# Optimization experiments

Measured on AMD Instinct MI355X. Metric: run time of the kernel, lower is better.

Reference implementation:

```python
import jax, jax.numpy as jnp
import numpy as np

B, T, D_MODEL, H = 4, 2048, 1024, 16
D_HEAD = D_MODEL // H
THETA = 10000.0


def setup_inputs() -> dict:
    key = jax.random.key(0)
    ks = jax.random.split(key, 5)
    s = 0.02
    return {
        "x": jax.random.normal(ks[0], (B, T, D_MODEL), dtype=jnp.float32),
        "Wq": jax.random.normal(ks[1], (D_MODEL, D_MODEL), dtype=jnp.float32) * s,
        "bq": jnp.zeros((D_MODEL,), dtype=jnp.float32),
        "Wk": jax.random.normal(ks[2], (D_MODEL, D_MODEL), dtype=jnp.float32) * s,
        "bk": jnp.zeros((D_MODEL,), dtype=jnp.float32),
        "Wv": jax.random.normal(ks[3], (D_MODEL, D_MODEL), dtype=jnp.float32) * s,
        "bv": jnp.zeros((D_MODEL,), dtype=jnp.float32),
        "Wo": jax.random.normal(ks[4], (D_MODEL, D_MODEL), dtype=jnp.float32) * s,
        "bo": jnp.zeros((D_MODEL,), dtype=jnp.float32),
    }


def _rope_tables(t_len, d_head, theta):
    inv_freq = 1.0 / theta ** (jnp.arange(0, d_head, 2, dtype=jnp.float32) / d_head)
    t = jnp.arange(t_len, dtype=jnp.float32)
    freqs = jnp.einsum('i,k->ik', t, inv_freq)  # [T, d_head/2]
    return jnp.cos(freqs), jnp.sin(freqs)


def _apply_rope(x, cos, sin):
    # x: [B, H, T, d_head]; cos/sin: [T, d_head/2] broadcast over B,H
    c = cos[None, None, :, :]
    s = sin[None, None, :, :]
    x0, x1 = x[..., ::2], x[..., 1::2]
    x_rot = jnp.stack((x0 * c - x1 * s, x0 * s + x1 * c), axis=-1)
    return x_rot.reshape(x.shape)


def reference(x, Wq, bq, Wk, bk, Wv, bv, Wo, bo):
    b, t, c = x.shape
    h, dh = H, D_HEAD
    q = (x @ Wq.T + bq).reshape(b, t, h, dh).transpose(0, 2, 1, 3)
    k = (x @ Wk.T + bk).reshape(b, t, h, dh).transpose(0, 2, 1, 3)
    v = (x @ Wv.T + bv).reshape(b, t, h, dh).transpose(0, 2, 1, 3)
    cos, sin = _rope_tables(t, dh, THETA)
    q = _apply_rope(q, cos, sin)
    k = _apply_rope(k, cos, sin)
    scores = jnp.einsum('bhqd,bhkd->bhqk', q, k) / jnp.sqrt(jnp.float32(dh))
    causal = jnp.tril(jnp.ones((t, t), dtype=bool))
    scores = jnp.where(causal[None, None, :, :], scores, -jnp.inf)
    attn = jax.nn.softmax(scores, axis=-1)
    out = jnp.einsum('bhqk,bhkd->bhqd', attn, v)
    out = out.transpose(0, 2, 1, 3).reshape(b, t, c)
    return out @ Wo.T + bo
```

## Files before the change

### kernel.cpp

```cpp
#include <hip/hip_runtime.h>
#include <hip/hip_bf16.h>

#define DEV static __device__ __forceinline__
#define AS1q __attribute__((address_space(1)))
#define AS3q __attribute__((address_space(3)))

typedef __attribute__((ext_vector_type(4))) float f32x4;
typedef __attribute__((ext_vector_type(16))) float f32x16;
typedef __attribute__((ext_vector_type(8))) short short8;
typedef __attribute__((ext_vector_type(4))) unsigned short u16x4;
typedef __attribute__((ext_vector_type(4))) unsigned int u32x4;

#define NB 4
#define NT 2048
#define NDM 1024
#define NH 16
#define NDH 64
#define NM (NB * NT)

DEV float bf2f(unsigned short u) {
  union { unsigned int i; float f; } x;
  x.i = ((unsigned int)u) << 16;
  return x.f;
}
DEV unsigned short f2bf(float f) {
  __hip_bfloat16 h = __float2bfloat16(f);
  return *reinterpret_cast<unsigned short*>(&h);
}
DEV unsigned int pack2bf(float lo, float hi) {
  return ((unsigned int)f2bf(hi) << 16) | (unsigned int)f2bf(lo);
}
DEV short8 mkfrag(unsigned int w0, unsigned int w1, unsigned int w2, unsigned int w3) {
  union { u32x4 u; short8 s; } x;
  x.u[0] = w0; x.u[1] = w1; x.u[2] = w2; x.u[3] = w3;
  return x.s;
}
DEV void permswap(unsigned int& a, unsigned int& b) {
  auto r = __builtin_amdgcn_permlane32_swap(a, b, false, false);
  a = r[0]; b = r[1];
}
DEV float dpp_swap1(float v) {
  union { float f; int i; } x; x.f = v;
  int r = __builtin_amdgcn_update_dpp(0, x.i, 0xB1, 0xF, 0xF, true);
  union { int i; float f; } y; y.i = r;
  return y.f;
}

__global__ __launch_bounds__(256) void k_cvt_bf16(const float* __restrict__ in,
                                                  unsigned short* __restrict__ out,
                                                  int n8) {
  int i = blockIdx.x * 256 + threadIdx.x;
  if (i >= n8) return;
  const f32x4* p = (const f32x4*)(in + (size_t)i * 8);
  f32x4 a = p[0], b = p[1];
  short8 o;
  o[0] = (short)f2bf(a[0]); o[1] = (short)f2bf(a[1]);
  o[2] = (short)f2bf(a[2]); o[3] = (short)f2bf(a[3]);
  o[4] = (short)f2bf(b[0]); o[5] = (short)f2bf(b[1]);
  o[6] = (short)f2bf(b[2]); o[7] = (short)f2bf(b[3]);
  *(short8*)(out + (size_t)i * 8) = o;
}

__global__ __launch_bounds__(256) void k_cvt_w(const float* __restrict__ w0, const float* __restrict__ w1,
                                               const float* __restrict__ w2, const float* __restrict__ w3,
                                               unsigned short* __restrict__ o0, unsigned short* __restrict__ o1,
                                               unsigned short* __restrict__ o2, unsigned short* __restrict__ o3) {
  int i = blockIdx.x * 256 + threadIdx.x;
  int m = blockIdx.y;
  const float* in = (m == 0) ? w0 : (m == 1) ? w1 : (m == 2) ? w2 : w3;
  unsigned short* out = (m == 0) ? o0 : (m == 1) ? o1 : (m == 2) ? o2 : o3;
  const f32x4* p = (const f32x4*)(in + (size_t)i * 8);
  f32x4 a = p[0], b = p[1];
  short8 o;
  o[0] = (short)f2bf(a[0]); o[1] = (short)f2bf(a[1]);
  o[2] = (short)f2bf(a[2]); o[3] = (short)f2bf(a[3]);
  o[4] = (short)f2bf(b[0]); o[5] = (short)f2bf(b[1]);
  o[6] = (short)f2bf(b[2]); o[7] = (short)f2bf(b[3]);
  *(short8*)(out + (size_t)i * 8) = o;
}

__global__ __launch_bounds__(256) void k_rope_table(float2* __restrict__ tab) {
  int i = blockIdx.x * 256 + threadIdx.x;
  int t = i >> 5, f = i & 31;
  float inv = powf(10000.0f, -(float)f / 32.0f);
  float ang = (float)t * inv;
  tab[i] = make_float2(cosf(ang), sinf(ang));
}

DEV void gemm_core(const unsigned short* __restrict__ Ab,
                   const unsigned short* __restrict__ Bb,
                   int Kdim, unsigned short* lds,
                   int tid, int wr, int wc, int lq, int gg,
                   f32x4 (&acc)[4][4]) {
  const int c0 = tid,       r0 = c0 >> 2; const int o0 = ((c0 & 3) ^ ((r0 >> 2) & 3)) * 8;
  const int c1 = tid + 256, r1 = c1 >> 2; const int o1 = ((c1 & 3) ^ ((r1 >> 2) & 3)) * 8;
  const unsigned short* pa0 = Ab + (size_t)r0 * Kdim + o0;
  const unsigned short* pa1 = Ab + (size_t)r1 * Kdim + o1;
  const unsigned short* pb0 = Bb + (size_t)r0 * Kdim + o0;
  const unsigned short* pb1 = Bb + (size_t)r1 * Kdim + o1;
  const int e0 = c0 * 8, e1 = c1 * 8;

  auto stage = [&](int buf, int ko) {
    unsigned short* LA = lds + buf * 4096;
    unsigned short* LB = lds + 8192 + buf * 4096;
    __builtin_amdgcn_global_load_lds((const AS1q void*)(pa0 + ko), (AS3q void*)(LA + e0), 16, 0, 0);
    __builtin_amdgcn_global_load_lds((const AS1q void*)(pa1 + ko), (AS3q void*)(LA + e1), 16, 0, 0);
    __builtin_amdgcn_global_load_lds((const AS1q void*)(pb0 + ko), (AS3q void*)(LB + e0), 16, 0, 0);
    __builtin_amdgcn_global_load_lds((const AS1q void*)(pb1 + ko), (AS3q void*)(LB + e1), 16, 0, 0);
  };

  const int rowA = (wr + lq) * 32, rowB = (wc + lq) * 32;
  const int cAB = ((gg ^ ((lq >> 2) & 3)) & 3) * 8;

  const int NKT = Kdim >> 5;
  stage(0, 0);
  __syncthreads();
  int cur = 0;
  for (int t = 0; t < NKT; ++t) {
    if (t + 1 < NKT) stage(cur ^ 1, (t + 1) << 5);
    const unsigned short* LA = lds + cur * 4096;
    const unsigned short* LB = lds + 8192 + cur * 4096;
    short8 af[4], bf[4];
#pragma unroll
    for (int i = 0; i < 4; ++i) af[i] = *(const short8*)&LA[rowA + i * 512 + cAB];
#pragma unroll
    for (int j = 0; j < 4; ++j) bf[j] = *(const short8*)&LB[rowB + j * 512 + cAB];
#pragma unroll
    for (int i = 0; i < 4; ++i)
#pragma unroll
      for (int j = 0; j < 4; ++j)
        acc[i][j] = __builtin_amdgcn_mfma_f32_16x16x32_bf16(af[i], bf[j], acc[i][j], 0, 0, 0);
    __syncthreads();
    cur ^= 1;
  }
}

__global__ __launch_bounds__(256) void k_gemm_qkv(const unsigned short* __restrict__ A,
                                                  const unsigned short* __restrict__ Bw,
                                                  const float* __restrict__ bq,
                                                  const float* __restrict__ bk,
                                                  const float* __restrict__ bv,
                                                  const float2* __restrict__ tab,
                                                  unsigned short* __restrict__ QH,
                                                  unsigned short* __restrict__ KH,
                                                  unsigned short* __restrict__ VT) {
  __shared__ unsigned short lds[4 * 4096];
  const int K = NDM;
  const int tid = threadIdx.x;
  const int lane = tid & 63;
  const int wave = tid >> 6;
  const int wr = (wave >> 1) * 64;
  const int wc = (wave & 1) * 64;
  const int lq = lane & 15;
  const int gg = lane >> 4;

  unsigned int nbx = gridDim.x;
  unsigned int bid = blockIdx.y * nbx + blockIdx.x;
  unsigned int cpx = (nbx * gridDim.y) >> 3;
  unsigned int swz = (bid & 7) * cpx + (bid >> 3);
  const int bn = swz % nbx, bm = swz / nbx;

  const unsigned short* Ab = A + (size_t)bm * 128 * K;
  const unsigned short* Bb = Bw + (size_t)bn * 128 * K;

  f32x4 acc[4][4] = {};
  gemm_core(Ab, Bb, K, lds, tid, wr, wc, lq, gg, acc);

  const int which = bn >> 3;
  const int nloc = (bn & 7) * 128;
  const int rowb = bm * 128 + wr + (lane >> 4) * 4;
  const int colb = nloc + wc + lq;

  if (which == 2) {
#pragma unroll
    for (int i = 0; i < 4; ++i) {
#pragma unroll
      for (int j = 0; j < 4; ++j) {
        const int col = colb + j * 16;
        const float bs = bv[col];
        const int h = col >> 6, dh = col & 63;
        u16x4 w;
#pragma unroll
        for (int r = 0; r < 4; ++r) w[r] = f2bf(acc[i][j][r] + bs);
        const int row = rowb + i * 16;
        const int bb = row >> 11, t = row & (NT - 1);
        *(u16x4*)&VT[(((size_t)(bb * NH + h)) * NDH + dh) * NT + t] = w;
      }
    }
  } else {
    const float* bias = which ? bk : bq;
    unsigned short* Out = which ? KH : QH;
    const float sc = which ? 1.0f : 0.125f * 1.44269504088896f;
#pragma unroll
    for (int i = 0; i < 4; ++i) {
#pragma unroll
      for (int j = 0; j < 4; ++j) {
        const int col = colb + j * 16;
        const float bs = bias[col];
        const int h = col >> 6, dh = col & 63;
        const int pidx = dh >> 1;
        const bool odd = dh & 1;
#pragma unroll
        for (int r = 0; r < 4; ++r) {
          const int row = rowb + i * 16 + r;
          const int bb = row >> 11, t = row & (NT - 1);
          const float v = acc[i][j][r] + bs;
          const float pv = dpp_swap1(v);
          const float2 cs = tab[t * 32 + pidx];
          const float y = odd ? (pv * cs.y + v * cs.x) : (v * cs.x - pv * cs.y);
          Out[(((size_t)(bb * NH + h)) * NT + t) * NDH + dh] = f2bf(y * sc);
        }
      }
    }
  }
}

__global__ __launch_bounds__(256) void k_gemm_bt(const unsigned short* __restrict__ A,
                                                 const unsigned short* __restrict__ Bw,
                                                 const float* __restrict__ bias,
                                                 float* __restrict__ Cout,
                                                 int M, int N, int K) {
  __shared__ unsigned short lds[4 * 4096];
  const int tid = threadIdx.x;
  const int lane = tid & 63;
  const int wave = tid >> 6;
  const int wr = (wave >> 1) * 64;
  const int wc = (wave & 1) * 64;
  const int lq = lane & 15;
  const int gg = lane >> 4;

  unsigned int nbx = gridDim.x;
  unsigned int bid = blockIdx.y * nbx + blockIdx.x;
  unsigned int cpx = (nbx * gridDim.y) >> 3;
  unsigned int swz = (bid & 7) * cpx + (bid >> 3);
  const int bn = swz % nbx, bm = swz / nbx;

  const unsigned short* Ab = A + (size_t)bm * 128 * K;
  const unsigned short* Bb = Bw + (size_t)bn * 128 * K;

  f32x4 acc[4][4] = {};
  gemm_core(Ab, Bb, K, lds, tid, wr, wc, lq, gg, acc);

  const int rowb = bm * 128 + wr + (lane >> 4) * 4;
  const int colb = bn * 128 + wc + lq;
#pragma unroll
  for (int i = 0; i < 4; ++i) {
#pragma unroll
    for (int j = 0; j < 4; ++j) {
      const int col = colb + j * 16;
      const float bs = bias[col];
#pragma unroll
      for (int r = 0; r < 4; ++r) {
        const size_t idx = (size_t)(rowb + i * 16 + r) * N + col;
        Cout[idx] = acc[i][j][r] + bs;
      }
    }
  }
}

__global__ __launch_bounds__(256, 2) void k_attn(const unsigned short* __restrict__ Qh,
                                                 const unsigned short* __restrict__ Kh,
                                                 const unsigned short* __restrict__ Vtp,
                                                 unsigned short* __restrict__ Ctx) {
  __shared__ unsigned short kl[2][64 * 64];
  __shared__ unsigned short vl[2][64 * 64];
  const int tid = threadIdx.x;
  const int wave = tid >> 6, lane = tid & 63;
  const int l31 = lane & 31, hi = lane >> 5;
  const int b0 = blockIdx.x;
  const int bh = (b0 & 7) * 8 + ((b0 >> 3) & 7);
  const int t = 15 - (b0 >> 6);
  const int b = bh >> 4, h = bh & 15;

  const unsigned short* K = Kh + (size_t)bh * NT * NDH;
  const unsigned short* V = Vtp + (size_t)bh * NDH * NT;

  const int ch0 = tid, ch1 = tid + 256;
  const int sr0 = ch0 >> 3, sc0 = ((ch0 & 7) ^ (sr0 & 7)) * 8;
  const int sr1 = ch1 >> 3, sc1 = ((ch1 & 7) ^ (sr1 & 7)) * 8;
  const int xe = (l31 & 7) << 3;

  auto stage = [&](int buf, int kv0) {
    __builtin_amdgcn_global_load_lds(
        (const AS1q void*)(K + (size_t)(kv0 + sr0) * NDH + sc0),
        (AS3q void*)(&kl[buf][ch0 * 8]), 16, 0, 0);
    __builtin_amdgcn_global_load_lds(
        (const AS1q void*)(K + (size_t)(kv0 + sr1) * NDH + sc1),
        (AS3q void*)(&kl[buf][ch1 * 8]), 16, 0, 0);
    __builtin_amdgcn_global_load_lds(
        (const AS1q void*)(V + (size_t)sr0 * NT + kv0 + sc0),
        (AS3q void*)(&vl[buf][ch0 * 8]), 16, 0, 0);
    __builtin_amdgcn_global_load_lds(
        (const AS1q void*)(V + (size_t)sr1 * NT + kv0 + sc1),
        (AS3q void*)(&vl[buf][ch1 * 8]), 16, 0, 0);
  };

  const int q0w = t * 128 + wave * 32;
  const int nkv = 2 * t + 2;

  const unsigned short* Qr = Qh + ((size_t)bh * NT + q0w + l31) * NDH + 8 * hi;
  short8 qf[4];
#pragma unroll
  for (int s = 0; s < 4; ++s) qf[s] = *(const short8*)&Qr[16 * s];

  short8 onesf;
#pragma unroll
  for (int s = 0; s < 8; ++s) onesf[s] = (short)0x3F80;

  f32x16 ot0 = {}, ot1 = {}, lacc = {};

  stage(0, 0);
  __syncthreads();

  for (int kb = 0; kb < nkv; ++kb) {
    const int cur = kb & 1;
    const int kv0 = kb * 64;
    if (kb + 1 < nkv) stage(cur ^ 1, kv0 + 64);

    if (kv0 <= q0w + 31) {
      const unsigned short* kc = kl[cur];
      f32x16 st0 = {}, st1 = {};
      __builtin_amdgcn_s_setprio(1);
#pragma unroll
      for (int s = 0; s < 4; ++s) {
        const int co = (16 * s + 8 * hi) ^ xe;
        short8 k0 = *(const short8*)&kc[l31 * 64 + co];
        short8 k1 = *(const short8*)&kc[(32 + l31) * 64 + co];
        st0 = __builtin_amdgcn_mfma_f32_32x32x16_bf16(k0, qf[s], st0, 0, 0, 0);
        st1 = __builtin_amdgcn_mfma_f32_32x32x16_bf16(k1, qf[s], st1, 0, 0, 0);
      }
      __builtin_amdgcn_s_setprio(0);
      if (kv0 + 64 > q0w) {
        const int qg = q0w + l31;
#pragma unroll
        for (int r = 0; r < 16; ++r) {
          const int kr = kv0 + (r & 3) + 8 * (r >> 2) + 4 * hi;
          if (kr > qg) st0[r] = -1e30f;
          if (kr + 32 > qg) st1[r] = -1e30f;
        }
      }
#pragma unroll
      for (int r = 0; r < 16; ++r) st0[r] = exp2f(st0[r]);
#pragma unroll
      for (int r = 0; r < 16; ++r) st1[r] = exp2f(st1[r]);
      short8 pf[4];
#pragma unroll
      for (int ks = 0; ks < 4; ++ks) {
        const f32x16& sm = (ks & 2) ? st1 : st0;
        const int o = (ks & 1) * 8;
        unsigned int w0 = pack2bf(sm[o + 0], sm[o + 1]);
        unsigned int w2 = pack2bf(sm[o + 4], sm[o + 5]);
        permswap(w0, w2);
        unsigned int w1 = pack2bf(sm[o + 2], sm[o + 3]);
        unsigned int w3 = pack2bf(sm[o + 6], sm[o + 7]);
        permswap(w1, w3);
        pf[ks] = mkfrag(w0, w1, w2, w3);
      }
      const unsigned short* vc = vl[cur];
      __builtin_amdgcn_s_setprio(1);
#pragma unroll
      for (int ks = 0; ks < 4; ++ks) {
        const int co = (16 * ks + 8 * hi) ^ xe;
        short8 v0 = *(const short8*)&vc[l31 * 64 + co];
        short8 v1 = *(const short8*)&vc[(32 + l31) * 64 + co];
        ot0 = __builtin_amdgcn_mfma_f32_32x32x16_bf16(v0, pf[ks], ot0, 0, 0, 0);
        ot1 = __builtin_amdgcn_mfma_f32_32x32x16_bf16(v1, pf[ks], ot1, 0, 0, 0);
        lacc = __builtin_amdgcn_mfma_f32_32x32x16_bf16(onesf, pf[ks], lacc, 0, 0, 0);
      }
      __builtin_amdgcn_s_setprio(0);
    }
    __syncthreads();
  }

  const float inv_l = 1.0f / lacc[0];
  unsigned short* dst = Ctx + ((size_t)(b * NT) + q0w + l31) * NDM + h * NDH;
#pragma unroll
  for (int dt = 0; dt < 2; ++dt) {
#pragma unroll
    for (int grp = 0; grp < 4; ++grp) {
      u16x4 w;
#pragma unroll
      for (int r = 0; r < 4; ++r) {
        const float v = (dt ? ot1[grp * 4 + r] : ot0[grp * 4 + r]) * inv_l;
        w[r] = f2bf(v);
      }
      *(u16x4*)&dst[dt * 32 + grp * 8 + 4 * hi] = w;
    }
  }
}

extern "C" void kernel_launch(void* const* d_in, const int* in_sizes, int n_in,
                              void* d_out, int out_size, void* d_ws, size_t ws_size,
                              hipStream_t stream) {
  const float* x  = (const float*)d_in[0];
  const float* Wq = (const float*)d_in[1];
  const float* bq = (const float*)d_in[2];
  const float* Wk = (const float*)d_in[3];
  const float* bk = (const float*)d_in[4];
  const float* Wv = (const float*)d_in[5];
  const float* bv = (const float*)d_in[6];
  const float* Wo = (const float*)d_in[7];
  const float* bo = (const float*)d_in[8];

  char* ws = (char*)d_ws;
  const size_t MB = 1024 * 1024;
  if (ws_size < 90 * MB) return;

  unsigned short* XB   = (unsigned short*)(ws + 0);
  unsigned short* WQB  = (unsigned short*)(ws + 16 * MB);
  unsigned short* WKB  = (unsigned short*)(ws + 18 * MB);
  unsigned short* WVB  = (unsigned short*)(ws + 20 * MB);
  unsigned short* WOB  = (unsigned short*)(ws + 22 * MB);
  unsigned short* QH   = (unsigned short*)(ws + 24 * MB);
  unsigned short* KH   = (unsigned short*)(ws + 40 * MB);
  unsigned short* VT   = (unsigned short*)(ws + 56 * MB);
  unsigned short* CTX  = (unsigned short*)(ws + 72 * MB);
  float2* TAB          = (float2*)(ws + 88 * MB);

  k_cvt_bf16<<<(NM * NDM / 8) / 256, 256, 0, stream>>>(x, XB, NM * NDM / 8);
  dim3 gw((NDM * NDM / 8) / 256, 4);
  k_cvt_w<<<gw, 256, 0, stream>>>(Wq, Wk, Wv, Wo, WQB, WKB, WVB, WOB);
  k_rope_table<<<(NT * 32) / 256, 256, 0, stream>>>(TAB);

  dim3 gq(3 * NDM / 128, NM / 128);
  k_gemm_qkv<<<gq, 256, 0, stream>>>(XB, WQB, bq, bk, bv, TAB, QH, KH, VT);

  k_attn<<<NB * NH * 16, 256, 0, stream>>>(QH, KH, VT, CTX);

  dim3 go(NDM / 128, NM / 128);
  k_gemm_bt<<<go, 256, 0, stream>>>(CTX, WOB, bo, (float*)d_out, NM, NDM, NDM);
}
```

Before: 194.4 us.

## Enlarge projection GEMM tiles to 128x256 with 8 waves and BK=64

Replaces the 128x128 tile, 4-wave GEMM core used by the QKV and output projections with a 128x256 tile, 8-wave core that walks K in steps of 64 and uses an 8-way XOR LDS swizzle. The pipeline waits with explicit vmcnt and raw s_barrier instead of __syncthreads, and raises wave priority around the MFMA blocks. The goal is better operand reuse per LDS byte and fewer K iterations and barriers. The cost is more LDS per block (96 KB) and fewer blocks in the grid, which may lower occupancy and the wave count per CU.

```diff
diff --git a/kernel.cpp b/kernel.cpp
--- a/kernel.cpp
+++ b/kernel.cpp
@@ -87,55 +87,86 @@
   tab[i] = make_float2(cosf(ang), sinf(ang));
 }
 
-DEV void gemm_core(const unsigned short* __restrict__ Ab,
-                   const unsigned short* __restrict__ Bb,
-                   int Kdim, unsigned short* lds,
-                   int tid, int wr, int wc, int lq, int gg,
-                   f32x4 (&acc)[4][4]) {
-  const int c0 = tid,       r0 = c0 >> 2; const int o0 = ((c0 & 3) ^ ((r0 >> 2) & 3)) * 8;
-  const int c1 = tid + 256, r1 = c1 >> 2; const int o1 = ((c1 & 3) ^ ((r1 >> 2) & 3)) * 8;
-  const unsigned short* pa0 = Ab + (size_t)r0 * Kdim + o0;
-  const unsigned short* pa1 = Ab + (size_t)r1 * Kdim + o1;
-  const unsigned short* pb0 = Bb + (size_t)r0 * Kdim + o0;
-  const unsigned short* pb1 = Bb + (size_t)r1 * Kdim + o1;
-  const int e0 = c0 * 8, e1 = c1 * 8;
+DEV void gemm256_core(const unsigned short* __restrict__ Ab,
+                      const unsigned short* __restrict__ Bb,
+                      int Kdim, unsigned short* lds,
+                      int tid, int wm, int wn, int lq, int gg,
+                      f32x4 (&acc)[4][4]) {
+  const int ca0 = tid,        ra0 = ca0 >> 3; const int oa0 = ((ca0 & 7) ^ (ra0 & 7)) * 8;
+  const int ca1 = tid + 512,  ra1 = ca1 >> 3; const int oa1 = ((ca1 & 7) ^ (ra1 & 7)) * 8;
+  const int cb0 = tid,        rb0 = cb0 >> 3; const int ob0 = ((cb0 & 7) ^ (rb0 & 7)) * 8;
+  const int cb1 = tid + 512,  rb1 = cb1 >> 3; const int ob1 = ((cb1 & 7) ^ (rb1 & 7)) * 8;
+  const int cb2 = tid + 1024, rb2 = cb2 >> 3; const int ob2 = ((cb2 & 7) ^ (rb2 & 7)) * 8;
+  const int cb3 = tid + 1536, rb3 = cb3 >> 3; const int ob3 = ((cb3 & 7) ^ (rb3 & 7)) * 8;
+  const unsigned short* pa0 = Ab + (size_t)ra0 * Kdim + oa0;
+  const unsigned short* pa1 = Ab + (size_t)ra1 * Kdim + oa1;
+  const unsigned short* pb0 = Bb + (size_t)rb0 * Kdim + ob0;
+  const unsigned short* pb1 = Bb + (size_t)rb1 * Kdim + ob1;
+  const unsigned short* pb2 = Bb + (size_t)rb2 * Kdim + ob2;
+  const unsigned short* pb3 = Bb + (size_t)rb3 * Kdim + ob3;
+  const int ea0 = ca0 * 8, ea1 = ca1 * 8;
+  const int eb0 = cb0 * 8, eb1 = cb1 * 8, eb2 = cb2 * 8, eb3 = cb3 * 8;
 
   auto stage = [&](int buf, int ko) {
-    unsigned short* LA = lds + buf * 4096;
-    unsigned short* LB = lds + 8192 + buf * 4096;
-    __builtin_amdgcn_global_load_lds((const AS1q void*)(pa0 + ko), (AS3q void*)(LA + e0), 16, 0, 0);
-    __builtin_amdgcn_global_load_lds((const AS1q void*)(pa1 + ko), (AS3q void*)(LA + e1), 16, 0, 0);
-    __builtin_amdgcn_global_load_lds((const AS1q void*)(pb0 + ko), (AS3q void*)(LB + e0), 16, 0, 0);
-    __builtin_amdgcn_global_load_lds((const AS1q void*)(pb1 + ko), (AS3q void*)(LB + e1), 16, 0, 0);
+    unsigned short* LA = lds + buf * 8192;
+    unsigned short* LB = lds + 16384 + buf * 16384;
+    __builtin_amdgcn_global_load_lds((const AS1q void*)(pa0 + ko), (AS3q void*)(LA + ea0), 16, 0, 0);
+    __builtin_amdgcn_global_load_lds((const AS1q void*)(pa1 + ko), (AS3q void*)(LA + ea1), 16, 0, 0);
+    __builtin_amdgcn_global_load_lds((const AS1q void*)(pb0 + ko), (AS3q void*)(LB + eb0), 16, 0, 0);
+    __builtin_amdgcn_global_load_lds((const AS1q void*)(pb1 + ko), (AS3q void*)(LB + eb1), 16, 0, 0);
+    __builtin_amdgcn_global_load_lds((const AS1q void*)(pb2 + ko), (AS3q void*)(LB + eb2), 16, 0, 0);
+    __builtin_amdgcn_global_load_lds((const AS1q void*)(pb3 + ko), (AS3q void*)(LB + eb3), 16, 0, 0);
   };
 
-  const int rowA = (wr + lq) * 32, rowB = (wc + lq) * 32;
-  const int cAB = ((gg ^ ((lq >> 2) & 3)) & 3) * 8;
-
-  const int NKT = Kdim >> 5;
+  const int xr = lq & 7;
+  const int rA = (wm * 64 + lq) * 64;
+  const int rB = (wn * 64 + lq) * 64;
+  const int c0 = (gg ^ xr) * 8;
+  const int c1 = ((4 + gg) ^ xr) * 8;
+
+  const int NKT = Kdim >> 6;
   stage(0, 0);
-  __syncthreads();
-  int cur = 0;
   for (int t = 0; t < NKT; ++t) {
-    if (t + 1 < NKT) stage(cur ^ 1, (t + 1) << 5);
-    const unsigned short* LA = lds + cur * 4096;
-    const unsigned short* LB = lds + 8192 + cur * 4096;
+    if (t + 1 < NKT) {
+      stage((t + 1) & 1, (t + 1) << 6);
+      asm volatile("s_waitcnt vmcnt(6)" ::: "memory");
+    } else {
+      asm volatile("s_waitcnt vmcnt(0)" ::: "memory");
+    }
+    __builtin_amdgcn_s_barrier();
+    __builtin_amdgcn_sched_barrier(0);
+    const unsigned short* LA = lds + (t & 1) * 8192;
+    const unsigned short* LB = lds + 16384 + (t & 1) * 16384;
     short8 af[4], bf[4];
 #pragma unroll
-    for (int i = 0; i < 4; ++i) af[i] = *(const short8*)&LA[rowA + i * 512 + cAB];
-#pragma unroll
-    for (int j = 0; j < 4; ++j) bf[j] = *(const short8*)&LB[rowB + j * 512 + cAB];
-#pragma unroll
-    for (int i = 0; i < 4; ++i)
-#pragma unroll
-      for (int j = 0; j < 4; ++j)
-        acc[i][j] = __builtin_amdgcn_mfma_f32_16x16x32_bf16(af[i], bf[j], acc[i][j], 0, 0, 0);
-    __syncthreads();
-    cur ^= 1;
+    for (int m = 0; m < 4; ++m) af[m] = *(const short8*)&LA[rA + m * 1024 + c0];
+#pragma unroll
+    for (int n = 0; n < 4; ++n) bf[n] = *(const short8*)&LB[rB + n * 1024 + c0];
+    __builtin_amdgcn_s_setprio(1);
+#pragma unroll
+    for (int m = 0; m < 4; ++m)
+#pragma unroll
+      for (int n = 0; n < 4; ++n)
+        acc[m][n] = __builtin_amdgcn_mfma_f32_16x16x32_bf16(af[m], bf[n], acc[m][n], 0, 0, 0);
+    __builtin_amdgcn_s_setprio(0);
+#pragma unroll
+    for (int m = 0; m < 4; ++m) af[m] = *(const short8*)&LA[rA + m * 1024 + c1];
+#pragma unroll
+    for (int n = 0; n < 4; ++n) bf[n] = *(const short8*)&LB[rB + n * 1024 + c1];
+    __builtin_amdgcn_s_setprio(1);
+#pragma unroll
+    for (int m = 0; m < 4; ++m)
+#pragma unroll
+      for (int n = 0; n < 4; ++n)
+        acc[m][n] = __builtin_amdgcn_mfma_f32_16x16x32_bf16(af[m], bf[n], acc[m][n], 0, 0, 0);
+    __builtin_amdgcn_s_setprio(0);
+    asm volatile("s_waitcnt lgkmcnt(0)" ::: "memory");
+    __builtin_amdgcn_sched_barrier(0);
+    __builtin_amdgcn_s_barrier();
   }
 }
 
-__global__ __launch_bounds__(256) void k_gemm_qkv(const unsigned short* __restrict__ A,
+__global__ __launch_bounds__(512) void k_gemm_qkv(const unsigned short* __restrict__ A,
                                                   const unsigned short* __restrict__ Bw,
                                                   const float* __restrict__ bq,
                                                   const float* __restrict__ bk,
@@ -144,13 +175,12 @@
                                                   unsigned short* __restrict__ QH,
                                                   unsigned short* __restrict__ KH,
                                                   unsigned short* __restrict__ VT) {
-  __shared__ unsigned short lds[4 * 4096];
+  __shared__ unsigned short lds[49152];
   const int K = NDM;
   const int tid = threadIdx.x;
   const int lane = tid & 63;
-  const int wave = tid >> 6;
-  const int wr = (wave >> 1) * 64;
-  const int wc = (wave & 1) * 64;
+  const int wid = tid >> 6;
+  const int wm = wid >> 2, wn = wid & 3;
   const int lq = lane & 15;
   const int gg = lane >> 4;
 
@@ -161,15 +191,14 @@
   const int bn = swz % nbx, bm = swz / nbx;
 
   const unsigned short* Ab = A + (size_t)bm * 128 * K;
-  const unsigned short* Bb = Bw + (size_t)bn * 128 * K;
+  const unsigned short* Bb = Bw + (size_t)bn * 256 * K;
 
   f32x4 acc[4][4] = {};
-  gemm_core(Ab, Bb, K, lds, tid, wr, wc, lq, gg, acc);
-
-  const int which = bn >> 3;
-  const int nloc = (bn & 7) * 128;
-  const int rowb = bm * 128 + wr + (lane >> 4) * 4;
-  const int colb = nloc + wc + lq;
+  gemm256_core(Ab, Bb, K, lds, tid, wm, wn, lq, gg, acc);
+
+  const int which = bn >> 2;
+  const int rowb = bm * 128 + wm * 64 + gg * 4;
+  const int colb = (bn & 3) * 256 + wn * 64 + lq;
 
   if (which == 2) {
 #pragma unroll
@@ -215,17 +244,16 @@
   }
 }
 
-__global__ __launch_bounds__(256) void k_gemm_bt(const unsigned short* __restrict__ A,
+__global__ __launch_bounds__(512) void k_gemm_bt(const unsigned short* __restrict__ A,
                                                  const unsigned short* __restrict__ Bw,
                                                  const float* __restrict__ bias,
                                                  float* __restrict__ Cout,
                                                  int M, int N, int K) {
-  __shared__ unsigned short lds[4 * 4096];
+  __shared__ unsigned short lds[49152];
   const int tid = threadIdx.x;
   const int lane = tid & 63;
-  const int wave = tid >> 6;
-  const int wr = (wave >> 1) * 64;
-  const int wc = (wave & 1) * 64;
+  const int wid = tid >> 6;
+  const int wm = wid >> 2, wn = wid & 3;
   const int lq = lane & 15;
   const int gg = lane >> 4;
 
@@ -236,13 +264,13 @@
   const int bn = swz % nbx, bm = swz / nbx;
 
   const unsigned short* Ab = A + (size_t)bm * 128 * K;
-  const unsigned short* Bb = Bw + (size_t)bn * 128 * K;
+  const unsigned short* Bb = Bw + (size_t)bn * 256 * K;
 
   f32x4 acc[4][4] = {};
-  gemm_core(Ab, Bb, K, lds, tid, wr, wc, lq, gg, acc);
-
-  const int rowb = bm * 128 + wr + (lane >> 4) * 4;
-  const int colb = bn * 128 + wc + lq;
+  gemm256_core(Ab, Bb, K, lds, tid, wm, wn, lq, gg, acc);
+
+  const int rowb = bm * 128 + wm * 64 + gg * 4;
+  const int colb = bn * 256 + wn * 64 + lq;
 #pragma unroll
   for (int i = 0; i < 4; ++i) {
 #pragma unroll
@@ -422,11 +450,11 @@
   k_cvt_w<<<gw, 256, 0, stream>>>(Wq, Wk, Wv, Wo, WQB, WKB, WVB, WOB);
   k_rope_table<<<(NT * 32) / 256, 256, 0, stream>>>(TAB);
 
-  dim3 gq(3 * NDM / 128, NM / 128);
-  k_gemm_qkv<<<gq, 256, 0, stream>>>(XB, WQB, bq, bk, bv, TAB, QH, KH, VT);
+  dim3 gq(3 * NDM / 256, NM / 128);
+  k_gemm_qkv<<<gq, 512, 0, stream>>>(XB, WQB, bq, bk, bv, TAB, QH, KH, VT);
 
   k_attn<<<NB * NH * 16, 256, 0, stream>>>(QH, KH, VT, CTX);
 
-  dim3 go(NDM / 128, NM / 128);
-  k_gemm_bt<<<go, 256, 0, stream>>>(CTX, WOB, bo, (float*)d_out, NM, NDM, NDM);
-}
+  dim3 go(NDM / 256, NM / 128);
+  k_gemm_bt<<<go, 512, 0, stream>>>(CTX, WOB, bo, (float*)d_out, NM, NDM, NDM);
+}
```

After: 184.1 us. -5.3%, faster.
